# Optimization experiments

Measured on AMD Instinct MI355X. Metric: run time of the kernel, lower is better.

The kernel has to match this reference:

```python
import jax, jax.numpy as jnp
import numpy as np

IN_DIM, D, H, L = 2, 256, 8, 3
FF = 4 * D
PAST, FUT, B = 50, 20, 128
S = PAST + FUT
DH = D // H
EPS = 1e-5


def setup_inputs() -> dict:
    key = jax.random.key(0)
    ks = jax.random.split(key, 12)
    def w(k, shape, s=0.02):
        return jax.random.normal(k, shape, dtype=jnp.float32) * s
    return dict(
        past_trajectory=jax.random.normal(ks[0], (B, PAST, IN_DIM), dtype=jnp.float32),
        in_W=w(ks[1], (D, IN_DIM), 0.5), in_b=jnp.zeros((D,), jnp.float32),
        pos_emb=w(ks[2], (S, D), 1.0),
        ln0_w=jnp.ones((D,), jnp.float32), ln0_b=jnp.zeros((D,), jnp.float32),
        sa_Wqkv=w(ks[3], (L, 3 * D, D)), sa_bqkv=jnp.zeros((L, 3 * D), jnp.float32),
        sa_Wo=w(ks[4], (L, D, D)), sa_bo=jnp.zeros((L, D), jnp.float32),
        ca_Wqkv=w(ks[5], (L, 3 * D, D)), ca_bqkv=jnp.zeros((L, 3 * D), jnp.float32),
        ca_Wo=w(ks[6], (L, D, D)), ca_bo=jnp.zeros((L, D), jnp.float32),
        ff1_W=w(ks[7], (L, FF, D)), ff1_b=jnp.zeros((L, FF), jnp.float32),
        ff2_W=w(ks[8], (L, D, FF)), ff2_b=jnp.zeros((L, D), jnp.float32),
        ln1_w=jnp.ones((L, D), jnp.float32), ln1_b=jnp.zeros((L, D), jnp.float32),
        ln2_w=jnp.ones((L, D), jnp.float32), ln2_b=jnp.zeros((L, D), jnp.float32),
        ln3_w=jnp.ones((L, D), jnp.float32), ln3_b=jnp.zeros((L, D), jnp.float32),
        out_W=w(ks[9], (IN_DIM, D), 0.5), out_b=jnp.zeros((IN_DIM,), jnp.float32),
    )


def _ln(x, wt, bias):
    m = x.mean(-1, keepdims=True)
    v = ((x - m) ** 2).mean(-1, keepdims=True)  # biased var, as torch LayerNorm
    return (x - m) * jax.lax.rsqrt(v + EPS) * wt + bias


def _mha(q_in, kv_in, Wqkv, bqkv, Wo, bo, neg_mask):
    # torch nn.MultiheadAttention: packed in_proj [3D, D], y = x @ W.T + b
    Wq, Wk, Wv = Wqkv[:D], Wqkv[D:2 * D], Wqkv[2 * D:]
    bq, bk, bv = bqkv[:D], bqkv[D:2 * D], bqkv[2 * D:]
    b, s = q_in.shape[0], q_in.shape[1]
    q = (q_in @ Wq.T + bq).reshape(b, s, H, DH)
    k = (kv_in @ Wk.T + bk).reshape(b, s, H, DH)
    v = (kv_in @ Wv.T + bv).reshape(b, s, H, DH)
    scores = jnp.einsum('bqhd,bkhd->bhqk', q, k) * (1.0 / np.sqrt(DH))
    attn = jax.nn.softmax(scores + neg_mask, axis=-1)
    out = jnp.einsum('bhqk,bkhd->bqhd', attn, v).reshape(b, s, D)
    return out @ Wo.T + bo


def reference(past_trajectory, in_W, in_b, pos_emb, ln0_w, ln0_b,
              sa_Wqkv, sa_bqkv, sa_Wo, sa_bo, ca_Wqkv, ca_bqkv, ca_Wo, ca_bo,
              ff1_W, ff1_b, ff2_W, ff2_b,
              ln1_w, ln1_b, ln2_w, ln2_b, ln3_w, ln3_b, out_W, out_b):
    b = past_trajectory.shape[0]
    # deltas: zeros at t=0, then first differences
    past_deltas = jnp.concatenate(
        [jnp.zeros_like(past_trajectory[:, :1]),
         past_trajectory[:, 1:] - past_trajectory[:, :-1]], axis=1)
    causal = jnp.triu(jnp.ones((S, S), jnp.bool_), 1)
    neg_mask = jnp.where(causal, jnp.float32(-1e9), jnp.float32(0.0))[None, None]

    def full_forward(full_deltas):
        # Causal mask makes row t depend only on deltas[:, :t+1], so running at
        # the fixed padded length S reproduces the original per-step re-encode.
        x = _ln(full_deltas @ in_W.T + in_b + pos_emb[None], ln0_w, ln0_b)
        mem = x  # TransformerDecoder memory stays fixed across layers
        for l in range(L):
            x = _ln(x + _mha(x, x, sa_Wqkv[l], sa_bqkv[l], sa_Wo[l], sa_bo[l], neg_mask), ln1_w[l], ln1_b[l])
            x = _ln(x + _mha(x, mem, ca_Wqkv[l], ca_bqkv[l], ca_Wo[l], ca_bo[l], neg_mask), ln2_w[l], ln2_b[l])
            h = jax.nn.gelu(x @ ff1_W[l].T + ff1_b[l], approximate=False)
            x = _ln(x + h @ ff2_W[l].T + ff2_b[l], ln3_w[l], ln3_b[l])
        return x

    def step(carry, s_idx):
        fd, cur = carry
        out = full_forward(jnp.concatenate([past_deltas, fd], axis=1))
        row = jnp.take(out, PAST + s_idx - 1, axis=1)  # last valid position
        nd = row @ out_W.T + out_b
        fd = fd.at[:, s_idx].set(nd)
        cur = cur + nd
        return (fd, cur), cur

    init = (jnp.zeros((b, FUT, IN_DIM), past_trajectory.dtype), past_trajectory[:, -1])
    _, pos = jax.lax.scan(step, init, jnp.arange(FUT))
    return jnp.transpose(pos, (1, 0, 2))  # (B, FUT, 2)
```

## Files before the change

kernel.cpp:

```cpp
#include <hip/hip_runtime.h>
#include <hip/hip_bf16.h>

#define DMODEL 256
#define S_TOT  70
#define BATCH  128
#define HEADS  8
#define DHEAD  32
#define PAST_N 50
#define FUT_N  20
#define LAYERS 3
#define FFD    1024

#define NT 512
#define SUBT_W   192
#define TOTAL_ENT (8 * SUBT_W * 256)

__device__ __forceinline__ float wave_sum64(float v) {
#pragma unroll
  for (int off = 32; off > 0; off >>= 1) v += __shfl_xor(v, off, 64);
  return v;
}
__device__ __forceinline__ float wave_max64(float v) {
#pragma unroll
  for (int off = 32; off > 0; off >>= 1) v = fmaxf(v, __shfl_xor(v, off, 64));
  return v;
}
__device__ __forceinline__ float gelu_f(float x) {
  return 0.5f * x * (1.0f + erff(x * 0.7071067811865476f));
}
__device__ __forceinline__ uint16_t f2bf(float v) {
  uint32_t b = __float_as_uint(v);
  return (uint16_t)((b + 0x7fffu + ((b >> 16) & 1u)) >> 16);
}
__device__ __forceinline__ float bl16(uint32_t w) { return __uint_as_float(w << 16); }
__device__ __forceinline__ float bh16(uint32_t w) { return __uint_as_float(w & 0xffff0000u); }
__device__ __forceinline__ uint16_t f2h(float v) {
  _Float16 h = (_Float16)v;
  return __builtin_bit_cast(uint16_t, h);
}
__device__ __forceinline__ uint32_t pk2(float lo_, float hi_) {
  return ((uint32_t)f2h(hi_) << 16) | (uint32_t)f2h(lo_);
}
__device__ __forceinline__ float fdot2a(uint32_t a, uint32_t b, float acc) {
  asm("v_dot2_f32_f16 %0, %1, %2, %0" : "+v"(acc) : "v"(a), "v"(b));
  return acc;
}

#define SYNC() do { __builtin_amdgcn_sched_barrier(0); \
  asm volatile("s_waitcnt lgkmcnt(0)" ::: "memory"); \
  __builtin_amdgcn_s_barrier(); \
  __builtin_amdgcn_sched_barrier(0); } while (0)
#define VMWAIT8() do { __builtin_amdgcn_sched_barrier(0); \
  asm volatile("s_waitcnt vmcnt(8)" ::: "memory"); \
  __builtin_amdgcn_sched_barrier(0); } while (0)

__device__ __forceinline__ void gld_lds16(const uint4* g, uint4* l) {
  __builtin_amdgcn_global_load_lds(
      (const __attribute__((address_space(1))) void*)g,
      (__attribute__((address_space(3))) void*)l, 16, 0, 0);
}

__device__ __forceinline__ float ln_norm_256(float x, float g, float b, float* sbuf, int tid) {
  float s = wave_sum64(x);
  if ((tid & 63) == 0) sbuf[tid >> 6] = s;
  __syncthreads();
  float mean = (sbuf[0] + sbuf[1] + sbuf[2] + sbuf[3]) * (1.0f / 256.0f);
  __syncthreads();
  float d = x - mean;
  float vs = wave_sum64(d * d);
  if ((tid & 63) == 0) sbuf[tid >> 6] = vs;
  __syncthreads();
  float var = (sbuf[0] + sbuf[1] + sbuf[2] + sbuf[3]) * (1.0f / 256.0f);
  return d * rsqrtf(var + 1e-5f) * g + b;
}

#define LDK 72

__global__ __launch_bounds__(256) void k_gemm_mf(
    const float* __restrict__ A, const float* __restrict__ W,
    const float* __restrict__ bias, const float* __restrict__ Rres,
    float* __restrict__ C, int M, int N, int K, int act, int outmode,
    float* __restrict__ qout, __hip_bfloat16* __restrict__ kc,
    __hip_bfloat16* __restrict__ vc, __hip_bfloat16* __restrict__ c6,
    int rows_per_b, int pos_base)
{
  typedef __attribute__((ext_vector_type(8))) short bf8;
  typedef __attribute__((ext_vector_type(4))) float f4;
  __shared__ short Al[2][128 * LDK];
  __shared__ short Bl[2][64 * LDK];
  const int tid = threadIdx.x;
  const int wv = tid >> 6, lane = tid & 63;
  const int bm0 = blockIdx.y * 128, bn0 = blockIdx.x * 64;
  const int nkt = K >> 6;
  const int ar = tid >> 1, ah = (tid & 1) << 5;
  const int br = tid >> 2, bq = (tid & 3) << 4;

  f4 acc[2][4];
#pragma unroll
  for (int i = 0; i < 2; i++)
#pragma unroll
    for (int j = 0; j < 4; j++) acc[i][j] = (f4)0.f;

  auto stage = [&](int buf, int kt) {
    const int k0 = kt << 6;
    const float* ap = A + (size_t)(bm0 + ar) * K + k0 + ah;
    float4 av[8];
#pragma unroll
    for (int u = 0; u < 8; u++) av[u] = *(const float4*)(ap + 4 * u);
    const float* wp = W + (size_t)(bn0 + br) * K + k0 + bq;
    float4 wv4[4];
#pragma unroll
    for (int u = 0; u < 4; u++) wv4[u] = *(const float4*)(wp + 4 * u);
    short* ad = &Al[buf][ar * LDK + ah];
#pragma unroll
    for (int u = 0; u < 8; u++) {
      short4 sv = {(short)f2bf(av[u].x), (short)f2bf(av[u].y),
                   (short)f2bf(av[u].z), (short)f2bf(av[u].w)};
      *(short4*)(ad + 4 * u) = sv;
    }
    short* bd = &Bl[buf][br * LDK + bq];
#pragma unroll
    for (int u = 0; u < 4; u++) {
      short4 sv = {(short)f2bf(wv4[u].x), (short)f2bf(wv4[u].y),
                   (short)f2bf(wv4[u].z), (short)f2bf(wv4[u].w)};
      *(short4*)(bd + 4 * u) = sv;
    }
  };

  auto comp = [&](int buf) {
    const int am = wv * 32 + (lane & 15);
    const int bn = lane & 15;
    const int kb = (lane >> 4) * 8;
#pragma unroll
    for (int kk = 0; kk < 2; kk++) {
      const int ko = kk * 32 + kb;
      bf8 a0 = *(const bf8*)&Al[buf][am * LDK + ko];
      bf8 a1 = *(const bf8*)&Al[buf][(am + 16) * LDK + ko];
      bf8 b0 = *(const bf8*)&Bl[buf][bn * LDK + ko];
      bf8 b1 = *(const bf8*)&Bl[buf][(bn + 16) * LDK + ko];
      bf8 b2 = *(const bf8*)&Bl[buf][(bn + 32) * LDK + ko];
      bf8 b3 = *(const bf8*)&Bl[buf][(bn + 48) * LDK + ko];
      acc[0][0] = __builtin_amdgcn_mfma_f32_16x16x32_bf16(a0, b0, acc[0][0], 0, 0, 0);
      acc[0][1] = __builtin_amdgcn_mfma_f32_16x16x32_bf16(a0, b1, acc[0][1], 0, 0, 0);
      acc[0][2] = __builtin_amdgcn_mfma_f32_16x16x32_bf16(a0, b2, acc[0][2], 0, 0, 0);
      acc[0][3] = __builtin_amdgcn_mfma_f32_16x16x32_bf16(a0, b3, acc[0][3], 0, 0, 0);
      acc[1][0] = __builtin_amdgcn_mfma_f32_16x16x32_bf16(a1, b0, acc[1][0], 0, 0, 0);
      acc[1][1] = __builtin_amdgcn_mfma_f32_16x16x32_bf16(a1, b1, acc[1][1], 0, 0, 0);
      acc[1][2] = __builtin_amdgcn_mfma_f32_16x16x32_bf16(a1, b2, acc[1][2], 0, 0, 0);
      acc[1][3] = __builtin_amdgcn_mfma_f32_16x16x32_bf16(a1, b3, acc[1][3], 0, 0, 0);
    }
  };

  stage(0, 0);
  __syncthreads();
  for (int kt = 0; kt < nkt; kt++) {
    if (kt + 1 < nkt) stage((kt & 1) ^ 1, kt + 1);
    comp(kt & 1);
    __syncthreads();
  }

  const int n0 = bn0 + (lane & 15);
  const int r0 = bm0 + wv * 32 + (lane >> 4) * 4;
#pragma unroll
  for (int i = 0; i < 2; i++) {
#pragma unroll
    for (int r = 0; r < 4; r++) {
      const int row = r0 + i * 16 + r;
      const int b = row / rows_per_b;
      const int t = pos_base + row % rows_per_b;
#pragma unroll
      for (int j = 0; j < 4; j++) {
        const int n = n0 + j * 16;
        float v = acc[i][j][r] + bias[n];
        if (Rres) v += Rres[(size_t)row * N + n];
        if (act) v = gelu_f(v);
        if (outmode == 0) {
          C[(size_t)row * N + n] = v;
        } else if (outmode == 1) {
          if (n < 256) qout[(size_t)row * DMODEL + n] = v;
          else if (n < 512) kc[((size_t)b * S_TOT + t) * DMODEL + (n - 256)] = __float2bfloat16(v);
          else vc[((size_t)b * S_TOT + t) * DMODEL + (n - 512)] = __float2bfloat16(v);
        } else {
          const int j6 = n >> 8;
          c6[(size_t)j6 * ((size_t)BATCH * S_TOT * DMODEL) +
             ((size_t)b * S_TOT + t) * DMODEL + (n & 255)] = __float2bfloat16(v);
        }
      }
    }
  }
}

__global__ __launch_bounds__(64) void k_attn(
    const float* __restrict__ qbuf, const __hip_bfloat16* __restrict__ kc,
    const __hip_bfloat16* __restrict__ vc, float* __restrict__ outb,
    int rows_per_b, int pos_base)
{
  __shared__ float qs[DHEAD];
  __shared__ float ss[S_TOT];
  const int bid = blockIdx.x;
  const int h = bid & (HEADS - 1);
  const int row = bid >> 3;
  const int b = row / rows_per_b;
  const int t = pos_base + row % rows_per_b;
  const int nk = t + 1;
  const int lane = threadIdx.x;
  if (lane < DHEAD) qs[lane] = qbuf[(size_t)row * DMODEL + h * DHEAD + lane];
  __syncthreads();
  float mx = -1e30f;
  for (int k0 = lane; k0 < nk; k0 += 64) {
    const __hip_bfloat16* kp = kc + ((size_t)b * S_TOT + k0) * DMODEL + h * DHEAD;
    float s = 0.f;
#pragma unroll
    for (int i = 0; i < DHEAD; i++) s += qs[i] * __bfloat162float(kp[i]);
    s *= 0.17677669529663687f;
    ss[k0] = s;
    mx = fmaxf(mx, s);
  }
  mx = wave_max64(mx);
  float sum = 0.f;
  for (int k0 = lane; k0 < nk; k0 += 64) {
    float e = expf(ss[k0] - mx);
    ss[k0] = e;
    sum += e;
  }
  sum = wave_sum64(sum);
  __syncthreads();
  const float inv = 1.0f / sum;
  if (lane < DHEAD) {
    float o = 0.f;
    for (int k0 = 0; k0 < nk; k0++)
      o += ss[k0] * __bfloat162float(vc[((size_t)b * S_TOT + k0) * DMODEL + h * DHEAD + lane]);
    outb[(size_t)row * DMODEL + h * DHEAD + lane] = o * inv;
  }
}

__global__ __launch_bounds__(256) void k_ln(
    const float* __restrict__ Z, const float* __restrict__ g,
    const float* __restrict__ b, float* __restrict__ out)
{
  __shared__ float sbuf[4];
  const int row = blockIdx.x, tid = threadIdx.x;
  float x = Z[(size_t)row * DMODEL + tid];
  out[(size_t)row * DMODEL + tid] = ln_norm_256(x, g[tid], b[tid], sbuf, tid);
}

__global__ __launch_bounds__(256) void k_embed(
    const float* __restrict__ past, const float* __restrict__ in_W,
    const float* __restrict__ in_b, const float* __restrict__ pos_emb,
    const float* __restrict__ ln_w, const float* __restrict__ ln_b,
    float* __restrict__ Aout)
{
  __shared__ float sbuf[4];
  const int rowid = blockIdx.x;
  const int b = rowid / PAST_N, t = rowid % PAST_N;
  const int tid = threadIdx.x;
  float dx = 0.f, dy = 0.f;
  if (t > 0) {
    dx = past[((size_t)b * PAST_N + t) * 2 + 0] - past[((size_t)b * PAST_N + t - 1) * 2 + 0];
    dy = past[((size_t)b * PAST_N + t) * 2 + 1] - past[((size_t)b * PAST_N + t - 1) * 2 + 1];
  }
  float v = in_W[tid * 2 + 0] * dx + in_W[tid * 2 + 1] * dy + in_b[tid] +
            pos_emb[(size_t)t * DMODEL + tid];
  Aout[(size_t)rowid * DMODEL + tid] = ln_norm_256(v, ln_w[tid], ln_b[tid], sbuf, tid);
}

__global__ __launch_bounds__(256) void k_prepack(
    const float* __restrict__ caW, const float* __restrict__ cab,
    float* __restrict__ Wckv, float* __restrict__ bckv)
{
  const int n = blockIdx.x, tid = threadIdx.x;
  const int j = n >> 8, dcol = n & 255;
  const int l = j >> 1, kv = j & 1;
  const int srow = l * 768 + 256 + kv * 256 + dcol;
  Wckv[(size_t)n * 256 + tid] = caW[(size_t)srow * 256 + tid];
  if (tid == 0) bckv[n] = cab[l * 768 + 256 + kv * 256 + dcol];
}

__global__ __launch_bounds__(64) void k_readout(
    const float* __restrict__ X, const float* __restrict__ out_W,
    const float* __restrict__ out_b, const float* __restrict__ past,
    float* __restrict__ cur, float* __restrict__ ndb, float* __restrict__ out,
    int rows_per_b, int s, int init)
{
  const int b = blockIdx.x, lane = threadIdx.x;
  const int row = b * rows_per_b + rows_per_b - 1;
  float p0 = 0.f, p1 = 0.f;
  for (int d = lane; d < DMODEL; d += 64) {
    const float xv = X[(size_t)row * DMODEL + d];
    p0 += xv * out_W[d];
    p1 += xv * out_W[DMODEL + d];
  }
  p0 = wave_sum64(p0);
  p1 = wave_sum64(p1);
  if (lane == 0) {
    const float nd0 = p0 + out_b[0];
    const float nd1 = p1 + out_b[1];
    float c0, c1;
    if (init) {
      c0 = past[((size_t)b * PAST_N + PAST_N - 1) * 2 + 0];
      c1 = past[((size_t)b * PAST_N + PAST_N - 1) * 2 + 1];
    } else {
      c0 = cur[b * 2 + 0];
      c1 = cur[b * 2 + 1];
    }
    c0 += nd0; c1 += nd1;
    cur[b * 2 + 0] = c0; cur[b * 2 + 1] = c1;
    ndb[b * 2 + 0] = nd0; ndb[b * 2 + 1] = nd1;
    out[((size_t)b * FUT_N + s) * 2 + 0] = c0;
    out[((size_t)b * FUT_N + s) * 2 + 1] = c1;
  }
}

__global__ __launch_bounds__(256) void k_pack_stream(
    const float* __restrict__ sa_Wqkv, const float* __restrict__ sa_Wo,
    const float* __restrict__ ca_Wqkv, const float* __restrict__ ca_Wo,
    const float* __restrict__ ff1_W, const float* __restrict__ ff2_W,
    uint4* __restrict__ Wd)
{
  const unsigned gidx = blockIdx.x * 256 + threadIdx.x;
  if (gidx >= TOTAL_ENT) return;
  const unsigned w = gidx / (SUBT_W * 256);
  const unsigned r = gidx % (SUBT_W * 256);
  const unsigned n = r >> 8, e = r & 255u;
  const int el = e & 63, ej = e >> 6;
  const int k8 = ((el >> 3) << 2) | ej;
  const int c = el & 7;
  const float* src;
  if (n < 24) {
    const int col = (int)(w * 8 + 64 * n + c);
    const int j6 = col >> 8, dcol = col & 255, lq = j6 >> 1, kv = j6 & 1;
    src = ca_Wqkv + (size_t)lq * 196608 + (size_t)(256 + kv * 256 + dcol) * 256 + 8 * k8;
  } else {
    const unsigned m = n - 24;
    const int l = m / 56, p = m % 56;
    if (p < 12)      { const int col = w * 8 + 64 * p + c;        src = sa_Wqkv + (size_t)l * 196608 + (size_t)col * 256 + 8 * k8; }
    else if (p < 16) { const int col = w * 8 + 64 * (p - 12) + c; src = sa_Wo   + (size_t)l * 65536  + (size_t)col * 256 + 8 * k8; }
    else if (p < 20) { const int col = w * 8 + 64 * (p - 16) + c; src = ca_Wqkv + (size_t)l * 196608 + (size_t)col * 256 + 8 * k8; }
    else if (p < 24) { const int col = w * 8 + 64 * (p - 20) + c; src = ca_Wo   + (size_t)l * 65536  + (size_t)col * 256 + 8 * k8; }
    else if (p < 40) { const int col = w * 8 + 64 * (p - 24) + c; src = ff1_W   + (size_t)l * 262144 + (size_t)col * 256 + 8 * k8; }
    else {
      const unsigned mm = p - 40;
      const int col = w * 8 + 64 * (mm >> 2) + c;
      const int kk8 = (int)(mm & 3) * 32 + k8;
      src = ff2_W + (size_t)l * 262144 + (size_t)col * 1024 + 8 * kk8;
    }
  }
  uint4 u;
  u.x = ((uint32_t)f2h(src[1]) << 16) | (uint32_t)f2h(src[0]);
  u.y = ((uint32_t)f2h(src[3]) << 16) | (uint32_t)f2h(src[2]);
  u.z = ((uint32_t)f2h(src[5]) << 16) | (uint32_t)f2h(src[4]);
  u.w = ((uint32_t)f2h(src[7]) << 16) | (uint32_t)f2h(src[6]);
  Wd[gidx] = u;
}

__global__ __launch_bounds__(NT) void k_decode(
    const uint4* __restrict__ Wd, const float* __restrict__ bckv,
    const float* __restrict__ in_W, const float* __restrict__ in_b,
    const float* __restrict__ pos_emb,
    const float* __restrict__ ln0_w, const float* __restrict__ ln0_b,
    const float* __restrict__ sa_bqkv, const float* __restrict__ sa_bo,
    const float* __restrict__ ca_bqkv, const float* __restrict__ ca_bo,
    const float* __restrict__ ff1_b, const float* __restrict__ ff2_b,
    const float* __restrict__ ln1_w, const float* __restrict__ ln1_b,
    const float* __restrict__ ln2_w, const float* __restrict__ ln2_b,
    const float* __restrict__ ln3_w, const float* __restrict__ ln3_b,
    const float* __restrict__ out_W, const float* __restrict__ out_b,
    __hip_bfloat16* __restrict__ Ksa, __hip_bfloat16* __restrict__ Vsa,
    __hip_bfloat16* __restrict__ C6,
    const float* __restrict__ ndb, const float* __restrict__ cur,
    float* __restrict__ out)
{
  const int b = blockIdx.x;
  const int tid = threadIdx.x;
  const int wv = tid >> 6, lane = tid & 63;
  const int sv = (wv + b) & 7;
  const size_t slab = (size_t)BATCH * S_TOT * DMODEL;

  __shared__ __align__(16) uint4 ring[8 * 4 * 256];
  __shared__ __align__(16) float x[256];
  __shared__ __align__(16) float xt[256];
  __shared__ __align__(16) float q[256];
  __shared__ __align__(16) float hbuf[1024];
  __shared__ __align__(16) float pred[256];
  __shared__ __align__(16) float kn[256], vn[256];
  __shared__ __align__(16) float ckvn[1536];
  __shared__ __align__(16) uint32_t xh[128], xth[128], atth[128], hh[512];
  __shared__ float ss[8][72];
  __shared__ float sb[8], sb2[8];
  __shared__ float ndc[4];

  const bool lo = tid < 256;
  const float c_bk0 = bckv[tid], c_bk1 = bckv[tid + 512], c_bk2 = bckv[tid + 1024];
  float c_inW0 = 0.f, c_inW1 = 0.f, c_inb = 0.f, c_l0w = 0.f, c_l0b = 0.f;
  if (lo) {
    c_inW0 = in_W[2 * tid]; c_inW1 = in_W[2 * tid + 1]; c_inb = in_b[tid];
    c_l0w = ln0_w[tid];     c_l0b = ln0_b[tid];
  }
  float bq0[LAYERS], bq1[LAYERS], bso[LAYERS], bcq[LAYERS], bco[LAYERS];
  float bf10[LAYERS], bf11[LAYERS], bf2[LAYERS];
  float w1[LAYERS], bb1[LAYERS], w2[LAYERS], bb2[LAYERS], w3[LAYERS], bb3[LAYERS];
#pragma unroll
  for (int l = 0; l < LAYERS; l++) {
    bq0[l] = sa_bqkv[l * 768 + tid];
    bq1[l] = lo ? sa_bqkv[l * 768 + 512 + tid] : 0.f;
    bso[l] = lo ? sa_bo[l * 256 + tid] : 0.f;
    bcq[l] = lo ? ca_bqkv[l * 768 + tid] : 0.f;
    bco[l] = lo ? ca_bo[l * 256 + tid] : 0.f;
    bf10[l] = ff1_b[l * 1024 + tid];
    bf11[l] = ff1_b[l * 1024 + 512 + tid];
    bf2[l] = lo ? ff2_b[l * 256 + tid] : 0.f;
    w1[l] = lo ? ln1_w[l * 256 + tid] : 0.f;  bb1[l] = lo ? ln1_b[l * 256 + tid] : 0.f;
    w2[l] = lo ? ln2_w[l * 256 + tid] : 0.f;  bb2[l] = lo ? ln2_b[l * 256 + tid] : 0.f;
    w3[l] = lo ? ln3_w[l * 256 + tid] : 0.f;  bb3[l] = lo ? ln3_b[l * 256 + tid] : 0.f;
  }
  float c_ow[4] = {0.f, 0.f, 0.f, 0.f};
  float c_ob = 0.f;
  if (tid < 128) {
    const int d0 = tid >> 6, ll = tid & 63;
#pragma unroll
    for (int j = 0; j < 4; j++) c_ow[j] = out_W[d0 * 256 + ll + 64 * j];
    c_ob = out_b[d0];
  }
  if (tid == 0) {
    ndc[0] = ndb[2 * b];     ndc[1] = ndb[2 * b + 1];
    ndc[2] = cur[2 * b];     ndc[3] = cur[2 * b + 1];
  }
  asm volatile("s_waitcnt vmcnt(0)" ::: "memory");

  auto issue = [&](unsigned g) {
    const unsigned sidx = g % (unsigned)SUBT_W;
    const unsigned slot = g & 3u;
    const uint4* src = Wd + (((size_t)sv * SUBT_W + sidx) << 8) + lane;
    uint4* dst = &ring[(((unsigned)wv << 2) | slot) * 256u + (unsigned)lane];
#pragma unroll
    for (int j = 0; j < 4; j++) gld_lds16(src + (j << 6), dst + (j << 6));
  };

  auto gemv1 = [&](unsigned& g, int cnt, const uint4* xp, auto&& emit) {
    const int kq = lane >> 3;
    const uint4 Xa = xp[kq * 4 + 0], Xb = xp[kq * 4 + 1];
    const uint4 Xc = xp[kq * 4 + 2], Xd = xp[kq * 4 + 3];
    for (int i = 0; i < cnt; i++) {
      VMWAIT8();
      issue(g + 3);
      const uint4* S = &ring[(((unsigned)wv << 2) | (g & 3u)) * 256u];
      const uint4 W0 = S[lane], W1 = S[64 + lane], W2 = S[128 + lane], W3 = S[192 + lane];
      float acc = 0.f;
      acc = fdot2a(W0.x, Xa.x, acc); acc = fdot2a(W0.y, Xa.y, acc);
      acc = fdot2a(W0.z, Xa.z, acc); acc = fdot2a(W0.w, Xa.w, acc);
      acc = fdot2a(W1.x, Xb.x, acc); acc = fdot2a(W1.y, Xb.y, acc);
      acc = fdot2a(W1.z, Xb.z, acc); acc = fdot2a(W1.w, Xb.w, acc);
      acc = fdot2a(W2.x, Xc.x, acc); acc = fdot2a(W2.y, Xc.y, acc);
      acc = fdot2a(W2.z, Xc.z, acc); acc = fdot2a(W2.w, Xc.w, acc);
      acc = fdot2a(W3.x, Xd.x, acc); acc = fdot2a(W3.y, Xd.y, acc);
      acc = fdot2a(W3.z, Xd.z, acc); acc = fdot2a(W3.w, Xd.w, acc);
      g++;
      acc += __shfl_xor(acc, 8, 64);
      acc += __shfl_xor(acc, 16, 64);
      acc += __shfl_xor(acc, 32, 64);
      if (lane < 8) emit((sv << 3) + (i << 6) + lane, acc);
    }
  };

  auto gemv4 = [&](unsigned& g, const uint4* xp, auto&& emit) {
    const int kq = lane >> 3;
    for (int i = 0; i < 4; i++) {
      float acc = 0.f;
      for (int kc = 0; kc < 4; kc++) {
        const uint4 Xa = xp[kc * 32 + kq * 4 + 0], Xb = xp[kc * 32 + kq * 4 + 1];
        const uint4 Xc = xp[kc * 32 + kq * 4 + 2], Xd = xp[kc * 32 + kq * 4 + 3];
        VMWAIT8();
        issue(g + 3);
        const uint4* S = &ring[(((unsigned)wv << 2) | (g & 3u)) * 256u];
        const uint4 W0 = S[lane], W1 = S[64 + lane], W2 = S[128 + lane], W3 = S[192 + lane];
        acc = fdot2a(W0.x, Xa.x, acc); acc = fdot2a(W0.y, Xa.y, acc);
        acc = fdot2a(W0.z, Xa.z, acc); acc = fdot2a(W0.w, Xa.w, acc);
        acc = fdot2a(W1.x, Xb.x, acc); acc = fdot2a(W1.y, Xb.y, acc);
        acc = fdot2a(W1.z, Xb.z, acc); acc = fdot2a(W1.w, Xb.w, acc);
        acc = fdot2a(W2.x, Xc.x, acc); acc = fdot2a(W2.y, Xc.y, acc);
        acc = fdot2a(W2.z, Xc.z, acc); acc = fdot2a(W2.w, Xc.w, acc);
        acc = fdot2a(W3.x, Xd.x, acc); acc = fdot2a(W3.y, Xd.y, acc);
        acc = fdot2a(W3.z, Xd.z, acc); acc = fdot2a(W3.w, Xd.w, acc);
        g++;
      }
      acc += __shfl_xor(acc, 8, 64);
      acc += __shfl_xor(acc, 16, 64);
      acc += __shfl_xor(acc, 32, 64);
      if (lane < 8) emit((sv << 3) + (i << 6) + lane, acc);
    }
  };

  auto ln_store = [&](float v, float gw_, float gb_, float* dst, uint32_t* dsth) {
    float vv = lo ? v : 0.f;
    float s  = wave_sum64(vv);
    float s2 = wave_sum64(vv * vv);
    if ((tid & 63) == 0) { sb[tid >> 6] = s; sb2[tid >> 6] = s2; }
    SYNC();
    float mean = (sb[0] + sb[1] + sb[2] + sb[3]) * (1.0f / 256.0f);
    float ex2  = (sb2[0] + sb2[1] + sb2[2] + sb2[3]) * (1.0f / 256.0f);
    float var = ex2 - mean * mean;
    float vn_ = (vv - mean) * rsqrtf(var + 1e-5f) * gw_ + gb_;
    float vo = __shfl_xor(vn_, 1, 64);
    if (lo) {
      dst[tid] = vn_;
      if (!(tid & 1)) dsth[tid >> 1] = pk2(vn_, vo);
    }
    SYNC();
  };

  auto attn8 = [&](const __hip_bfloat16* Kc, const __hip_bfloat16* Vc,
                   const float* knw, const float* vnw, int pos) {
    const int h = wv;
    const float* qh = q + h * 32;
    float mx = -1e30f;
    for (int k0 = lane; k0 <= pos; k0 += 64) {
      float s = 0.f;
      if (k0 == pos) {
        const float* kp = knw + h * 32;
#pragma unroll
        for (int i = 0; i < 32; i++) s += qh[i] * kp[i];
      } else {
        const uint32_t* kp = (const uint32_t*)(Kc + ((size_t)b * S_TOT + k0) * DMODEL + h * 32);
#pragma unroll
        for (int i = 0; i < 16; i++) {
          uint32_t w = kp[i];
          s += bl16(w) * qh[2 * i];
          s += bh16(w) * qh[2 * i + 1];
        }
      }
      s *= 0.17677669529663687f;
      ss[h][k0] = s;
      mx = fmaxf(mx, s);
    }
    mx = wave_max64(mx);
    float sum = 0.f;
    for (int k0 = lane; k0 <= pos; k0 += 64) {
      float e = __expf(ss[h][k0] - mx);
      ss[h][k0] = e;
      sum += e;
    }
    sum = wave_sum64(sum);
    const float inv = 1.0f / sum;
    const int kpar = lane >> 4, d2 = lane & 15;
    const uint32_t* vbase = (const uint32_t*)(Vc + (size_t)b * S_TOT * DMODEL + h * 32) + d2;
    float oA = 0.f, oB = 0.f;
    for (int k0 = kpar; k0 < pos; k0 += 4) {
      const uint32_t w = vbase[(size_t)k0 * (DMODEL / 2)];
      const float p = ss[h][k0];
      oA += p * bl16(w);
      oB += p * bh16(w);
    }
    oA += __shfl_xor(oA, 16, 64); oA += __shfl_xor(oA, 32, 64);
    oB += __shfl_xor(oB, 16, 64); oB += __shfl_xor(oB, 32, 64);
    if (kpar == 0) {
      const float p = ss[h][pos];
      oA += p * vnw[h * 32 + 2 * d2];
      oB += p * vnw[h * 32 + 2 * d2 + 1];
      atth[h * 16 + d2] = pk2(oA * inv, oB * inv);
    }
  };

  unsigned g = 0;
  issue(0); issue(1); issue(2);

  for (int s = 1; s < FUT_N; s++) {
    const int pos = PAST_N - 1 + s;

    float xe = 0.f;
    if (lo) {
      xe = c_inW0 * ndc[0] + c_inW1 * ndc[1] + c_inb + pos_emb[(size_t)pos * DMODEL + tid];
    }
    ln_store(xe, c_l0w, c_l0b, xt, xth);
    if (lo) x[tid] = xt[tid];
    if (tid < 128) xh[tid] = xth[tid];

    gemv1(g, 24, (const uint4*)xth, [&](int col, float a) { ckvn[col] = a; });
    SYNC();
    {
      float v0 = ckvn[tid] + c_bk0;
      float v1 = ckvn[tid + 512] + c_bk1;
      float v2 = ckvn[tid + 1024] + c_bk2;
      ckvn[tid] = v0; ckvn[tid + 512] = v1; ckvn[tid + 1024] = v2;
      int n = tid;
      C6[(size_t)(n >> 8) * slab + ((size_t)b * S_TOT + pos) * DMODEL + (n & 255)] = __float2bfloat16(v0);
      n = tid + 512;
      C6[(size_t)(n >> 8) * slab + ((size_t)b * S_TOT + pos) * DMODEL + (n & 255)] = __float2bfloat16(v1);
      n = tid + 1024;
      C6[(size_t)(n >> 8) * slab + ((size_t)b * S_TOT + pos) * DMODEL + (n & 255)] = __float2bfloat16(v2);
      SYNC();
    }

#pragma unroll
    for (int l = 0; l < LAYERS; l++) {
      gemv1(g, 12, (const uint4*)xh, [&](int col, float a) {
        if (col < 256) q[col] = a;
        else if (col < 512) kn[col - 256] = a;
        else vn[col - 512] = a;
      });
      SYNC();
      {
        if (tid < 256) q[tid] += bq0[l];
        else {
          float v2 = kn[tid - 256] + bq0[l];
          kn[tid - 256] = v2;
          Ksa[(size_t)l * slab + ((size_t)b * S_TOT + pos) * DMODEL + (tid - 256)] = __float2bfloat16(v2);
        }
        if (lo) {
          float v2 = vn[tid] + bq1[l];
          vn[tid] = v2;
          Vsa[(size_t)l * slab + ((size_t)b * S_TOT + pos) * DMODEL + tid] = __float2bfloat16(v2);
        }
        SYNC();
      }
      attn8(Ksa + (size_t)l * slab, Vsa + (size_t)l * slab, kn, vn, pos);
      SYNC();
      gemv1(g, 4, (const uint4*)atth, [&](int col, float a) { pred[col] = a; });
      SYNC();
      ln_store(lo ? (x[tid] + pred[tid] + bso[l]) : 0.f, w1[l], bb1[l], x, xh);
      gemv1(g, 4, (const uint4*)xh, [&](int col, float a) { pred[col] = a; });
      SYNC();
      if (lo) q[tid] = pred[tid] + bcq[l];
      SYNC();
      attn8(C6 + (size_t)(2 * l) * slab, C6 + (size_t)(2 * l + 1) * slab,
            ckvn + l * 512, ckvn + l * 512 + 256, pos);
      SYNC();
      gemv1(g, 4, (const uint4*)atth, [&](int col, float a) { pred[col] = a; });
      SYNC();
      ln_store(lo ? (x[tid] + pred[tid] + bco[l]) : 0.f, w2[l], bb2[l], x, xh);
      gemv1(g, 16, (const uint4*)xh, [&](int col, float a) { hbuf[col] = a; });
      SYNC();
      {
        float g0 = gelu_f(hbuf[tid] + bf10[l]);
        float g1 = gelu_f(hbuf[tid + 512] + bf11[l]);
        float o0 = __shfl_xor(g0, 1, 64), o1 = __shfl_xor(g1, 1, 64);
        if (!(tid & 1)) {
          hh[tid >> 1] = pk2(g0, o0);
          hh[(tid + 512) >> 1] = pk2(g1, o1);
        }
        SYNC();
      }
      gemv4(g, (const uint4*)hh, [&](int col, float a) { pred[col] = a; });
      SYNC();
      ln_store(lo ? (x[tid] + pred[tid] + bf2[l]) : 0.f, w3[l], bb3[l], x, xh);
    }

    {
      const int ll = tid & 63;
      if (tid < 128) {
        const int d0 = tid >> 6;
        float p = 0.f;
#pragma unroll
        for (int j = 0; j < 4; j++) p += x[ll + 64 * j] * c_ow[j];
        p = wave_sum64(p);
        if (ll == 0) {
          const float nd = p + c_ob;
          ndc[d0] = nd;
          const float c = ndc[2 + d0] + nd;
          ndc[2 + d0] = c;
          out[((size_t)b * FUT_N + s) * 2 + d0] = c;
        }
      }
      SYNC();
    }
  }
  asm volatile("s_waitcnt vmcnt(0)" ::: "memory");
}

extern "C" void kernel_launch(void* const* d_in, const int* in_sizes, int n_in,
                              void* d_out, int out_size, void* d_ws, size_t ws_size,
                              hipStream_t stream)
{
  const float* past    = (const float*)d_in[0];
  const float* in_W    = (const float*)d_in[1];
  const float* in_b    = (const float*)d_in[2];
  const float* pos_emb = (const float*)d_in[3];
  const float* ln0_w   = (const float*)d_in[4];
  const float* ln0_b   = (const float*)d_in[5];
  const float* sa_Wqkv = (const float*)d_in[6];
  const float* sa_bqkv = (const float*)d_in[7];
  const float* sa_Wo   = (const float*)d_in[8];
  const float* sa_bo   = (const float*)d_in[9];
  const float* ca_Wqkv = (const float*)d_in[10];
  const float* ca_bqkv = (const float*)d_in[11];
  const float* ca_Wo   = (const float*)d_in[12];
  const float* ca_bo   = (const float*)d_in[13];
  const float* ff1_W   = (const float*)d_in[14];
  const float* ff1_b   = (const float*)d_in[15];
  const float* ff2_W   = (const float*)d_in[16];
  const float* ff2_b   = (const float*)d_in[17];
  const float* ln1_w   = (const float*)d_in[18];
  const float* ln1_b   = (const float*)d_in[19];
  const float* ln2_w   = (const float*)d_in[20];
  const float* ln2_b   = (const float*)d_in[21];
  const float* ln3_w   = (const float*)d_in[22];
  const float* ln3_b   = (const float*)d_in[23];
  const float* out_W   = (const float*)d_in[24];
  const float* out_b   = (const float*)d_in[25];
  float* out = (float*)d_out;

  const size_t Mpre = (size_t)BATCH * PAST_N;
  const size_t slab = (size_t)BATCH * S_TOT * DMODEL;

  float* ws_f = (float*)d_ws;
  float* A    = ws_f;
  float* Bb   = A + Mpre * DMODEL;
  float* qb   = Bb + Mpre * DMODEL;
  float* at   = qb + Mpre * DMODEL;
  float* hb   = at + Mpre * DMODEL;
  float* Wckv = hb + Mpre * FFD;
  float* bckv = Wckv + (size_t)1536 * 256;
  float* ndb  = bckv + 1536;
  float* cur  = ndb + 256;
  __hip_bfloat16* Ksa = (__hip_bfloat16*)(cur + 256);
  __hip_bfloat16* Vsa = Ksa + 3 * slab;
  __hip_bfloat16* C6  = Vsa + 3 * slab;
  uint4* Wd = (uint4*)A;

  const size_t need = ((size_t)(C6 + 6 * slab) - (size_t)d_ws);
  if (ws_size < need) return;

  auto layer = [&](int l, int M, int rpb, int pbase) {
    const float* Wqkv = sa_Wqkv + (size_t)l * 768 * 256;
    __hip_bfloat16* kcl = Ksa + (size_t)l * slab;
    __hip_bfloat16* vcl = Vsa + (size_t)l * slab;
    k_gemm_mf<<<dim3(768 / 64, M / 128), 256, 0, stream>>>(
        A, Wqkv, sa_bqkv + l * 768, nullptr, nullptr, M, 768, 256, 0, 1,
        qb, kcl, vcl, nullptr, rpb, pbase);
    k_attn<<<M * HEADS, 64, 0, stream>>>(qb, kcl, vcl, at, rpb, pbase);
    k_gemm_mf<<<dim3(256 / 64, M / 128), 256, 0, stream>>>(
        at, sa_Wo + (size_t)l * 65536, sa_bo + l * 256, A, Bb, M, 256, 256, 0, 0,
        nullptr, nullptr, nullptr, nullptr, 1, 0);
    k_ln<<<M, 256, 0, stream>>>(Bb, ln1_w + l * 256, ln1_b + l * 256, A);
    k_gemm_mf<<<dim3(256 / 64, M / 128), 256, 0, stream>>>(
        A, ca_Wqkv + (size_t)l * 768 * 256, ca_bqkv + l * 768, nullptr, qb,
        M, 256, 256, 0, 0, nullptr, nullptr, nullptr, nullptr, 1, 0);
    k_attn<<<M * HEADS, 64, 0, stream>>>(
        qb, C6 + (size_t)(2 * l) * slab, C6 + (size_t)(2 * l + 1) * slab, at, rpb, pbase);
    k_gemm_mf<<<dim3(256 / 64, M / 128), 256, 0, stream>>>(
        at, ca_Wo + (size_t)l * 65536, ca_bo + l * 256, A, Bb, M, 256, 256, 0, 0,
        nullptr, nullptr, nullptr, nullptr, 1, 0);
    k_ln<<<M, 256, 0, stream>>>(Bb, ln2_w + l * 256, ln2_b + l * 256, A);
    k_gemm_mf<<<dim3(FFD / 64, M / 128), 256, 0, stream>>>(
        A, ff1_W + (size_t)l * FFD * 256, ff1_b + l * FFD, nullptr, hb,
        M, FFD, 256, 1, 0, nullptr, nullptr, nullptr, nullptr, 1, 0);
    k_gemm_mf<<<dim3(256 / 64, M / 128), 256, 0, stream>>>(
        hb, ff2_W + (size_t)l * 256 * FFD, ff2_b + l * 256, A, Bb, M, 256, FFD, 0, 0,
        nullptr, nullptr, nullptr, nullptr, 1, 0);
    k_ln<<<M, 256, 0, stream>>>(Bb, ln3_w + l * 256, ln3_b + l * 256, A);
  };

  k_prepack<<<1536, 256, 0, stream>>>(ca_Wqkv, ca_bqkv, Wckv, bckv);
  k_embed<<<(int)Mpre, 256, 0, stream>>>(past, in_W, in_b, pos_emb, ln0_w, ln0_b, A);
  k_gemm_mf<<<dim3(1536 / 64, (int)Mpre / 128), 256, 0, stream>>>(
      A, Wckv, bckv, nullptr, nullptr, (int)Mpre, 1536, 256, 0, 2,
      nullptr, nullptr, nullptr, C6, PAST_N, 0);
  for (int l = 0; l < LAYERS; l++) layer(l, (int)Mpre, PAST_N, 0);
  k_readout<<<BATCH, 64, 0, stream>>>(A, out_W, out_b, past, cur, ndb, out, PAST_N, 0, 1);

  k_pack_stream<<<(TOTAL_ENT + 255) / 256, 256, 0, stream>>>(
      sa_Wqkv, sa_Wo, ca_Wqkv, ca_Wo, ff1_W, ff2_W, Wd);

  k_decode<<<BATCH, NT, 0, stream>>>(
      Wd, bckv, in_W, in_b, pos_emb, ln0_w, ln0_b,
      sa_bqkv, sa_bo, ca_bqkv, ca_bo, ff1_b, ff2_b,
      ln1_w, ln1_b, ln2_w, ln2_b, ln3_w, ln3_b,
      out_W, out_b, Ksa, Vsa, C6, ndb, cur, out);
}
```

Before: 3.517 ms.

## Repack streamed weights so each wave owns contiguous 32-column blocks for GEMV

Changes the packed fp16 weight layout and GEMV so each lane handles one output column over half of K, with a 32-column block per wave instead of 8 strided columns. The per-output reduction drops from three cross-lane shuffles to one, and 32 lanes emit results instead of 8. The input-vector loads are now uniform across lanes within each K-half, which cuts LDS bank traffic but changes the LDS read pattern of the ring buffer. It also requires the output column mapping per wave (sv*width + cl) to stay consistent with the pack kernel.

```diff
diff --git a/kernel.cpp b/kernel.cpp
--- a/kernel.cpp
+++ b/kernel.cpp
@@ -322,27 +322,49 @@
   const unsigned w = gidx / (SUBT_W * 256);
   const unsigned r = gidx % (SUBT_W * 256);
   const unsigned n = r >> 8, e = r & 255u;
-  const int el = e & 63, ej = e >> 6;
-  const int k8 = ((el >> 3) << 2) | ej;
-  const int c = el & 7;
+  const int kh = e >> 7, j = (e >> 5) & 3, c = e & 31;
+  const int k8l = kh * 4 + j;
   const float* src;
   if (n < 24) {
-    const int col = (int)(w * 8 + 64 * n + c);
+    const int blk = n >> 2, st = n & 3;
+    const int col = (int)(w * 192 + blk * 32 + c);
+    const int k8 = st * 8 + k8l;
     const int j6 = col >> 8, dcol = col & 255, lq = j6 >> 1, kv = j6 & 1;
     src = ca_Wqkv + (size_t)lq * 196608 + (size_t)(256 + kv * 256 + dcol) * 256 + 8 * k8;
   } else {
     const unsigned m = n - 24;
     const int l = m / 56, p = m % 56;
-    if (p < 12)      { const int col = w * 8 + 64 * p + c;        src = sa_Wqkv + (size_t)l * 196608 + (size_t)col * 256 + 8 * k8; }
-    else if (p < 16) { const int col = w * 8 + 64 * (p - 12) + c; src = sa_Wo   + (size_t)l * 65536  + (size_t)col * 256 + 8 * k8; }
-    else if (p < 20) { const int col = w * 8 + 64 * (p - 16) + c; src = ca_Wqkv + (size_t)l * 196608 + (size_t)col * 256 + 8 * k8; }
-    else if (p < 24) { const int col = w * 8 + 64 * (p - 20) + c; src = ca_Wo   + (size_t)l * 65536  + (size_t)col * 256 + 8 * k8; }
-    else if (p < 40) { const int col = w * 8 + 64 * (p - 24) + c; src = ff1_W   + (size_t)l * 262144 + (size_t)col * 256 + 8 * k8; }
-    else {
-      const unsigned mm = p - 40;
-      const int col = w * 8 + 64 * (mm >> 2) + c;
-      const int kk8 = (int)(mm & 3) * 32 + k8;
-      src = ff2_W + (size_t)l * 262144 + (size_t)col * 1024 + 8 * kk8;
+    if (p < 12) {
+      const int blk = p >> 2, st = p & 3;
+      const int col = w * 96 + blk * 32 + c;
+      const int k8 = st * 8 + k8l;
+      src = sa_Wqkv + (size_t)l * 196608 + (size_t)col * 256 + 8 * k8;
+    } else if (p < 16) {
+      const int st = p - 12;
+      const int col = w * 32 + c;
+      const int k8 = st * 8 + k8l;
+      src = sa_Wo + (size_t)l * 65536 + (size_t)col * 256 + 8 * k8;
+    } else if (p < 20) {
+      const int st = p - 16;
+      const int col = w * 32 + c;
+      const int k8 = st * 8 + k8l;
+      src = ca_Wqkv + (size_t)l * 196608 + (size_t)col * 256 + 8 * k8;
+    } else if (p < 24) {
+      const int st = p - 20;
+      const int col = w * 32 + c;
+      const int k8 = st * 8 + k8l;
+      src = ca_Wo + (size_t)l * 65536 + (size_t)col * 256 + 8 * k8;
+    } else if (p < 40) {
+      const int pp = p - 24;
+      const int blk = pp >> 2, st = pp & 3;
+      const int col = w * 128 + blk * 32 + c;
+      const int k8 = st * 8 + k8l;
+      src = ff1_W + (size_t)l * 262144 + (size_t)col * 256 + 8 * k8;
+    } else {
+      const int st = p - 40;
+      const int col = w * 32 + c;
+      const int k8 = st * 8 + k8l;
+      src = ff2_W + (size_t)l * 262144 + (size_t)col * 1024 + 8 * k8;
     }
   }
   uint4 u;
@@ -436,57 +458,29 @@
     for (int j = 0; j < 4; j++) gld_lds16(src + (j << 6), dst + (j << 6));
   };
 
-  auto gemv1 = [&](unsigned& g, int cnt, const uint4* xp, auto&& emit) {
-    const int kq = lane >> 3;
-    const uint4 Xa = xp[kq * 4 + 0], Xb = xp[kq * 4 + 1];
-    const uint4 Xc = xp[kq * 4 + 2], Xd = xp[kq * 4 + 3];
-    for (int i = 0; i < cnt; i++) {
-      VMWAIT8();
-      issue(g + 3);
-      const uint4* S = &ring[(((unsigned)wv << 2) | (g & 3u)) * 256u];
-      const uint4 W0 = S[lane], W1 = S[64 + lane], W2 = S[128 + lane], W3 = S[192 + lane];
+  auto gemvB = [&](unsigned& g, int nblk, int nst, const uint4* xp, auto&& emit) {
+    const int kh = lane >> 5, c = lane & 31;
+    for (int bi = 0; bi < nblk; bi++) {
       float acc = 0.f;
-      acc = fdot2a(W0.x, Xa.x, acc); acc = fdot2a(W0.y, Xa.y, acc);
-      acc = fdot2a(W0.z, Xa.z, acc); acc = fdot2a(W0.w, Xa.w, acc);
-      acc = fdot2a(W1.x, Xb.x, acc); acc = fdot2a(W1.y, Xb.y, acc);
-      acc = fdot2a(W1.z, Xb.z, acc); acc = fdot2a(W1.w, Xb.w, acc);
-      acc = fdot2a(W2.x, Xc.x, acc); acc = fdot2a(W2.y, Xc.y, acc);
-      acc = fdot2a(W2.z, Xc.z, acc); acc = fdot2a(W2.w, Xc.w, acc);
-      acc = fdot2a(W3.x, Xd.x, acc); acc = fdot2a(W3.y, Xd.y, acc);
-      acc = fdot2a(W3.z, Xd.z, acc); acc = fdot2a(W3.w, Xd.w, acc);
-      g++;
-      acc += __shfl_xor(acc, 8, 64);
-      acc += __shfl_xor(acc, 16, 64);
-      acc += __shfl_xor(acc, 32, 64);
-      if (lane < 8) emit((sv << 3) + (i << 6) + lane, acc);
-    }
-  };
-
-  auto gemv4 = [&](unsigned& g, const uint4* xp, auto&& emit) {
-    const int kq = lane >> 3;
-    for (int i = 0; i < 4; i++) {
-      float acc = 0.f;
-      for (int kc = 0; kc < 4; kc++) {
-        const uint4 Xa = xp[kc * 32 + kq * 4 + 0], Xb = xp[kc * 32 + kq * 4 + 1];
-        const uint4 Xc = xp[kc * 32 + kq * 4 + 2], Xd = xp[kc * 32 + kq * 4 + 3];
+      for (int st = 0; st < nst; st++) {
         VMWAIT8();
         issue(g + 3);
-        const uint4* S = &ring[(((unsigned)wv << 2) | (g & 3u)) * 256u];
-        const uint4 W0 = S[lane], W1 = S[64 + lane], W2 = S[128 + lane], W3 = S[192 + lane];
-        acc = fdot2a(W0.x, Xa.x, acc); acc = fdot2a(W0.y, Xa.y, acc);
-        acc = fdot2a(W0.z, Xa.z, acc); acc = fdot2a(W0.w, Xa.w, acc);
-        acc = fdot2a(W1.x, Xb.x, acc); acc = fdot2a(W1.y, Xb.y, acc);
-        acc = fdot2a(W1.z, Xb.z, acc); acc = fdot2a(W1.w, Xb.w, acc);
-        acc = fdot2a(W2.x, Xc.x, acc); acc = fdot2a(W2.y, Xc.y, acc);
-        acc = fdot2a(W2.z, Xc.z, acc); acc = fdot2a(W2.w, Xc.w, acc);
-        acc = fdot2a(W3.x, Xd.x, acc); acc = fdot2a(W3.y, Xd.y, acc);
-        acc = fdot2a(W3.z, Xd.z, acc); acc = fdot2a(W3.w, Xd.w, acc);
+        const uint4* S = &ring[(((unsigned)wv << 2) | (g & 3u)) * 256u] + kh * 128 + c;
+        const uint4 W0 = S[0], W1 = S[32], W2 = S[64], W3 = S[96];
+        const int kb = st * 8 + kh * 4;
+        const uint4 X0 = xp[kb], X1 = xp[kb + 1], X2 = xp[kb + 2], X3 = xp[kb + 3];
+        acc = fdot2a(W0.x, X0.x, acc); acc = fdot2a(W0.y, X0.y, acc);
+        acc = fdot2a(W0.z, X0.z, acc); acc = fdot2a(W0.w, X0.w, acc);
+        acc = fdot2a(W1.x, X1.x, acc); acc = fdot2a(W1.y, X1.y, acc);
+        acc = fdot2a(W1.z, X1.z, acc); acc = fdot2a(W1.w, X1.w, acc);
+        acc = fdot2a(W2.x, X2.x, acc); acc = fdot2a(W2.y, X2.y, acc);
+        acc = fdot2a(W2.z, X2.z, acc); acc = fdot2a(W2.w, X2.w, acc);
+        acc = fdot2a(W3.x, X3.x, acc); acc = fdot2a(W3.y, X3.y, acc);
+        acc = fdot2a(W3.z, X3.z, acc); acc = fdot2a(W3.w, X3.w, acc);
         g++;
       }
-      acc += __shfl_xor(acc, 8, 64);
-      acc += __shfl_xor(acc, 16, 64);
       acc += __shfl_xor(acc, 32, 64);
-      if (lane < 8) emit((sv << 3) + (i << 6) + lane, acc);
+      if (lane < 32) emit(bi * 32 + c, acc);
     }
   };
 
@@ -574,7 +568,7 @@
     if (lo) x[tid] = xt[tid];
     if (tid < 128) xh[tid] = xth[tid];
 
-    gemv1(g, 24, (const uint4*)xth, [&](int col, float a) { ckvn[col] = a; });
+    gemvB(g, 6, 4, (const uint4*)xth, [&](int cl, float a) { ckvn[sv * 192 + cl] = a; });
     SYNC();
     {
       float v0 = ckvn[tid] + c_bk0;
@@ -592,7 +586,8 @@
 
 #pragma unroll
     for (int l = 0; l < LAYERS; l++) {
-      gemv1(g, 12, (const uint4*)xh, [&](int col, float a) {
+      gemvB(g, 3, 4, (const uint4*)xh, [&](int cl, float a) {
+        const int col = sv * 96 + cl;
         if (col < 256) q[col] = a;
         else if (col < 512) kn[col - 256] = a;
         else vn[col - 512] = a;
@@ -614,20 +609,20 @@
       }
       attn8(Ksa + (size_t)l * slab, Vsa + (size_t)l * slab, kn, vn, pos);
       SYNC();
-      gemv1(g, 4, (const uint4*)atth, [&](int col, float a) { pred[col] = a; });
+      gemvB(g, 1, 4, (const uint4*)atth, [&](int cl, float a) { pred[sv * 32 + cl] = a; });
       SYNC();
       ln_store(lo ? (x[tid] + pred[tid] + bso[l]) : 0.f, w1[l], bb1[l], x, xh);
-      gemv1(g, 4, (const uint4*)xh, [&](int col, float a) { pred[col] = a; });
+      gemvB(g, 1, 4, (const uint4*)xh, [&](int cl, float a) { pred[sv * 32 + cl] = a; });
       SYNC();
       if (lo) q[tid] = pred[tid] + bcq[l];
       SYNC();
       attn8(C6 + (size_t)(2 * l) * slab, C6 + (size_t)(2 * l + 1) * slab,
             ckvn + l * 512, ckvn + l * 512 + 256, pos);
       SYNC();
-      gemv1(g, 4, (const uint4*)atth, [&](int col, float a) { pred[col] = a; });
+      gemvB(g, 1, 4, (const uint4*)atth, [&](int cl, float a) { pred[sv * 32 + cl] = a; });
       SYNC();
       ln_store(lo ? (x[tid] + pred[tid] + bco[l]) : 0.f, w2[l], bb2[l], x, xh);
-      gemv1(g, 16, (const uint4*)xh, [&](int col, float a) { hbuf[col] = a; });
+      gemvB(g, 4, 4, (const uint4*)xh, [&](int cl, float a) { hbuf[sv * 128 + cl] = a; });
       SYNC();
       {
         float g0 = gelu_f(hbuf[tid] + bf10[l]);
@@ -639,7 +634,7 @@
         }
         SYNC();
       }
-      gemv4(g, (const uint4*)hh, [&](int col, float a) { pred[col] = a; });
+      gemvB(g, 1, 16, (const uint4*)hh, [&](int cl, float a) { pred[sv * 32 + cl] = a; });
       SYNC();
       ln_store(lo ? (x[tid] + pred[tid] + bf2[l]) : 0.f, w3[l], bb3[l], x, xh);
     }
```

Measured after the change: 3.426 ms (median of 2 runs). -2.6%, faster.
